# Optimization experiments

Hardware: AMD Instinct MI355X
Metric: run time of the kernel (lower is better)

## Reference

```python
import jax, jax.numpy as jnp
import numpy as np

HIDDEN = 1280
HEADS = 16
HEAD_DIM = HIDDEN // HEADS  # 80
B, N = 2, 2048


def _rotate_half(x):
    half = x.shape[-1] // 2
    return jnp.concatenate([-x[..., half:], x[..., :half]], axis=-1)


def setup_inputs() -> dict:
    key = jax.random.key(0)
    ks = jax.random.split(key, 7)
    x = jax.random.normal(ks[0], (B, N, HIDDEN), dtype=jnp.float32)
    cos = jax.random.uniform(ks[1], (N, HEAD_DIM), dtype=jnp.float32)
    sin = jax.random.uniform(ks[2], (N, HEAD_DIM), dtype=jnp.float32)
    s = 1.0 / np.sqrt(HIDDEN)
    qkv_w = jax.random.normal(ks[3], (HIDDEN, 3 * HIDDEN), dtype=jnp.float32) * s
    qkv_b = jax.random.normal(ks[4], (3 * HIDDEN,), dtype=jnp.float32) * 0.02
    proj_w = jax.random.normal(ks[5], (HIDDEN, HIDDEN), dtype=jnp.float32) * s
    proj_b = jax.random.normal(ks[6], (HIDDEN,), dtype=jnp.float32) * 0.02
    return {"x": x, "cos": cos, "sin": sin, "qkv_w": qkv_w, "qkv_b": qkv_b,
            "proj_w": proj_w, "proj_b": proj_b}


def reference(x, cos, sin, qkv_w, qkv_b, proj_w, proj_b):
    b, n, _ = x.shape
    scale = 1.0 / np.sqrt(HEAD_DIM).astype(np.float32)
    # fused QKV projection
    qkv = x @ qkv_w + qkv_b                                # [b, n, 3*hidden]
    qkv = qkv.reshape(b, n, 3, HEADS, HEAD_DIM)
    qkv = jnp.transpose(qkv, (2, 0, 3, 1, 4))              # [3, b, h, n, hd]
    q, k, v = qkv[0], qkv[1], qkv[2]
    # 2D RoPE
    cos_b = cos[None, None, :, :]
    sin_b = sin[None, None, :, :]
    q = q * cos_b + _rotate_half(q) * sin_b
    k = k * cos_b + _rotate_half(k) * sin_b
    # manual softmax attention
    scores = jnp.einsum('bhqd,bhkd->bhqk', q, k) * scale   # [b, h, n, n]
    attn = jax.nn.softmax(scores, axis=-1)
    out = jnp.einsum('bhqk,bhkd->bhqd', attn, v)           # [b, h, n, hd]
    out = jnp.transpose(out, (0, 2, 1, 3)).reshape(b, n, HIDDEN)
    return out @ proj_w + proj_b
```

## Files before the change

kernel.cpp:

```cpp
#include <hip/hip_runtime.h>
#include <hip/hip_bf16.h>
#include <math.h>

#define HIDDEN 1280
#define HEADS 16
#define HD 80
#define HALF 40
#define BB 2
#define NN 2048
#define MROWS (BB * NN)
#define QSCALE ((float)(0.11180339887498949 * 1.4426950408889634))

typedef __attribute__((ext_vector_type(8))) _Float16 f16x8;
typedef __attribute__((ext_vector_type(4))) float f32x4;

#define AS1 __attribute__((address_space(1)))
#define AS3 __attribute__((address_space(3)))

__device__ __forceinline__ void splitf16(float x, ushort& hi, ushort& lo) {
    _Float16 h = (_Float16)x;
    _Float16 l = (_Float16)(x - (float)h);
    hi = __builtin_bit_cast(ushort, h);
    lo = __builtin_bit_cast(ushort, l);
}

__device__ __forceinline__ ushort f2h(float x) {
    _Float16 h = (_Float16)x;
    return __builtin_bit_cast(ushort, h);
}

__global__ __launch_bounds__(256) void split_f16_kernel(
    const float* __restrict__ in, ushort* __restrict__ hi,
    ushort* __restrict__ lo, int n4)
{
    int i = blockIdx.x * 256 + threadIdx.x;
    if (i >= n4) return;
    float4 v = ((const float4*)in)[i];
    ushort4 h, l;
    splitf16(v.x, h.x, l.x);
    splitf16(v.y, h.y, l.y);
    splitf16(v.z, h.z, l.z);
    splitf16(v.w, h.w, l.w);
    ((ushort4*)hi)[i] = h;
    ((ushort4*)lo)[i] = l;
}

__global__ __launch_bounds__(256) void tsplit_f16_kernel(
    const float* __restrict__ W, ushort* __restrict__ T, int K, int N)
{
    __shared__ float s[32][33];
    const int n0 = blockIdx.x * 32;
    const int k0 = blockIdx.y * 32;
    {
        int tn = threadIdx.x & 31, tk = threadIdx.x >> 5;
        #pragma unroll
        for (int i = 0; i < 4; ++i)
            s[tk + i * 8][tn] = W[(size_t)(k0 + tk + i * 8) * N + n0 + tn];
    }
    __syncthreads();
    {
        int tk = threadIdx.x & 31, tn = threadIdx.x >> 5;
        #pragma unroll
        for (int i = 0; i < 4; ++i)
            T[(size_t)(n0 + tn + i * 8) * K + k0 + tk] = f2h(s[tk][tn + i * 8]);
    }
}

#define BM 128
#define BN 128
#define BK 32

__global__ __launch_bounds__(256) void gemm_f16x2_kernel(
    const ushort* __restrict__ Ahi, const ushort* __restrict__ Alo,
    const ushort* __restrict__ Bh,
    const float* __restrict__ bias, float* __restrict__ C,
    int M, int N, int K)
{
    __shared__ __align__(16) ushort lds[3 * 128 * 32];

    const int tid = threadIdx.x;
    const int wid = tid >> 6;
    const int lane = tid & 63;
    const int col0 = blockIdx.x * BN;
    const int row0 = blockIdx.y * BM;
    const int wy = wid >> 1, wx = wid & 1;
    const int lrow = lane >> 2;
    const int lchunk = lane & 3;

    f32x4 acc[4][4] = {};

    for (int k0 = 0; k0 < K; k0 += BK) {
        __syncthreads();
        #pragma unroll
        for (int i = 0; i < 6; ++i) {
            int s = wid + i * 4;
            int tile = s >> 3, t = s & 7;
            const ushort* src = (tile == 0) ? Ahi : (tile == 1) ? Alo : Bh;
            int srow = (tile < 2) ? row0 : col0;
            const ushort* g = src + (size_t)(srow + t * 16 + lrow) * K + k0 + lchunk * 8;
            ushort* l = lds + tile * 4096 + t * 512 + lane * 8;
            __builtin_amdgcn_global_load_lds(
                (const AS1 unsigned int*)g, (AS3 unsigned int*)l, 16, 0, 0);
        }
        __syncthreads();

        const int q = lane >> 4;
        const int r = lane & 15;
        f16x8 ah[4], al[4], bf[4];
        #pragma unroll
        for (int i = 0; i < 4; ++i) {
            int arow = wy * 64 + i * 16 + r;
            ah[i] = *(const f16x8*)(lds + 0 * 4096 + arow * 32 + q * 8);
            al[i] = *(const f16x8*)(lds + 1 * 4096 + arow * 32 + q * 8);
            int brow = wx * 64 + i * 16 + r;
            bf[i] = *(const f16x8*)(lds + 2 * 4096 + brow * 32 + q * 8);
        }
        #pragma unroll
        for (int i = 0; i < 4; ++i) {
            #pragma unroll
            for (int j = 0; j < 4; ++j) {
                acc[i][j] = __builtin_amdgcn_mfma_f32_16x16x32_f16(al[i], bf[j], acc[i][j], 0, 0, 0);
                acc[i][j] = __builtin_amdgcn_mfma_f32_16x16x32_f16(ah[i], bf[j], acc[i][j], 0, 0, 0);
            }
        }
    }

    const int q = lane >> 4, r = lane & 15;
    #pragma unroll
    for (int i = 0; i < 4; ++i) {
        #pragma unroll
        for (int j = 0; j < 4; ++j) {
            int col = col0 + wx * 64 + j * 16 + r;
            float b = bias[col];
            #pragma unroll
            for (int v = 0; v < 4; ++v) {
                int row = row0 + wy * 64 + i * 16 + q * 4 + v;
                C[(size_t)row * N + col] = acc[i][j][v] + b;
            }
        }
    }
}

__global__ __launch_bounds__(512, 2) void gemm_f16x2_256_kernel(
    const ushort* __restrict__ Ahi, const ushort* __restrict__ Alo,
    const ushort* __restrict__ Bh,
    const float* __restrict__ bias, float* __restrict__ C,
    int M, int N, int K, int nbx)
{
    __shared__ __align__(16) ushort lds[3 * 3 * 8192];

    const int tid = threadIdx.x;
    const int wid = tid >> 6;
    const int lane = tid & 63;
    const int q = lane >> 4, r = lane & 15;
    const int wr = wid >> 2, wc = wid & 3;

    int id = blockIdx.x;
    {
        int nwg = gridDim.x;
        if ((nwg & 7) == 0) {
            int c = nwg >> 3;
            id = (id & 7) * c + (id >> 3);
        }
    }
    const int row0 = (id / nbx) * 256;
    const int col0 = (id % nbx) * 256;

    const ushort* gsrc[6];
    int ldst[6];
    #pragma unroll
    for (int j = 0; j < 6; ++j) {
        int pj = j >> 1;
        int rloc = wid * 32 + (j & 1) * 16 + (lane >> 2);
        int sl = (lane & 3) ^ ((rloc >> 1) & 3);
        const ushort* base = (pj == 0) ? Ahi : (pj == 1) ? Alo : Bh;
        int grow = ((pj < 2) ? row0 : col0) + rloc;
        gsrc[j] = base + (size_t)grow * K + sl * 8;
        ldst[j] = pj * 8192 + (wid * 32 + (j & 1) * 16) * 32 + lane * 8;
    }

    const int NT = K / 32;

    #pragma unroll
    for (int j = 0; j < 6; ++j)
        __builtin_amdgcn_global_load_lds((const AS1 unsigned int*)(gsrc[j]),
            (AS3 unsigned int*)(lds + ldst[j]), 16, 0, 0);
    #pragma unroll
    for (int j = 0; j < 6; ++j)
        __builtin_amdgcn_global_load_lds((const AS1 unsigned int*)(gsrc[j] + 32),
            (AS3 unsigned int*)(lds + 24576 + ldst[j]), 16, 0, 0);
    asm volatile("s_waitcnt vmcnt(6)" ::: "memory");
    __builtin_amdgcn_s_barrier();

    const int soff = (q ^ ((r >> 1) & 3)) * 8;
    const int arow0 = wr * 128 + r;
    const int brow0 = wc * 64 + r;

    f32x4 acc[8][4] = {};
    f16x8 ah[4], al[4], bf[4];

    int cb = 0;
    int nb = 49152;

    for (int t = 0; t < NT; ++t) {
        const ushort* A0 = lds + cb;
        const ushort* A1 = lds + cb + 8192;
        const ushort* Bp = lds + cb + 16384;
        ushort* nbuf = lds + nb;
        const bool st = (t + 2 < NT);
        const int ko = (t + 2) * 32;

        #pragma unroll
        for (int m = 0; m < 4; ++m) {
            int ro = (arow0 + m * 16) * 32 + soff;
            ah[m] = *(const f16x8*)(A0 + ro);
            al[m] = *(const f16x8*)(A1 + ro);
        }
        #pragma unroll
        for (int n = 0; n < 2; ++n)
            bf[n] = *(const f16x8*)(Bp + (brow0 + n * 16) * 32 + soff);
        if (st) {
            __builtin_amdgcn_global_load_lds((const AS1 unsigned int*)(gsrc[0] + ko),
                (AS3 unsigned int*)(nbuf + ldst[0]), 16, 0, 0);
            __builtin_amdgcn_global_load_lds((const AS1 unsigned int*)(gsrc[1] + ko),
                (AS3 unsigned int*)(nbuf + ldst[1]), 16, 0, 0);
        }
        __builtin_amdgcn_s_barrier();
        asm volatile("s_waitcnt lgkmcnt(0)" ::: "memory");
        __builtin_amdgcn_sched_barrier(0);
        __builtin_amdgcn_s_setprio(1);
        #pragma unroll
        for (int m = 0; m < 4; ++m) {
            #pragma unroll
            for (int n = 0; n < 2; ++n) {
                acc[m][n] = __builtin_amdgcn_mfma_f32_16x16x32_f16(al[m], bf[n], acc[m][n], 0, 0, 0);
                acc[m][n] = __builtin_amdgcn_mfma_f32_16x16x32_f16(ah[m], bf[n], acc[m][n], 0, 0, 0);
            }
        }
        __builtin_amdgcn_s_setprio(0);
        __builtin_amdgcn_s_barrier();

        #pragma unroll
        for (int n = 2; n < 4; ++n)
            bf[n] = *(const f16x8*)(Bp + (brow0 + n * 16) * 32 + soff);
        if (st) {
            __builtin_amdgcn_global_load_lds((const AS1 unsigned int*)(gsrc[2] + ko),
                (AS3 unsigned int*)(nbuf + ldst[2]), 16, 0, 0);
            __builtin_amdgcn_global_load_lds((const AS1 unsigned int*)(gsrc[3] + ko),
                (AS3 unsigned int*)(nbuf + ldst[3]), 16, 0, 0);
        }
        __builtin_amdgcn_s_barrier();
        asm volatile("s_waitcnt lgkmcnt(0)" ::: "memory");
        __builtin_amdgcn_sched_barrier(0);
        __builtin_amdgcn_s_setprio(1);
        #pragma unroll
        for (int m = 0; m < 4; ++m) {
            #pragma unroll
            for (int n = 2; n < 4; ++n) {
                acc[m][n] = __builtin_amdgcn_mfma_f32_16x16x32_f16(al[m], bf[n], acc[m][n], 0, 0, 0);
                acc[m][n] = __builtin_amdgcn_mfma_f32_16x16x32_f16(ah[m], bf[n], acc[m][n], 0, 0, 0);
            }
        }
        __builtin_amdgcn_s_setprio(0);
        __builtin_amdgcn_s_barrier();

        #pragma unroll
        for (int m = 0; m < 4; ++m) {
            int ro = (arow0 + (m + 4) * 16) * 32 + soff;
            ah[m] = *(const f16x8*)(A0 + ro);
            al[m] = *(const f16x8*)(A1 + ro);
        }
        if (st) {
            __builtin_amdgcn_global_load_lds((const AS1 unsigned int*)(gsrc[4] + ko),
                (AS3 unsigned int*)(nbuf + ldst[4]), 16, 0, 0);
            __builtin_amdgcn_global_load_lds((const AS1 unsigned int*)(gsrc[5] + ko),
                (AS3 unsigned int*)(nbuf + ldst[5]), 16, 0, 0);
        }
        __builtin_amdgcn_s_barrier();
        asm volatile("s_waitcnt lgkmcnt(0)" ::: "memory");
        __builtin_amdgcn_sched_barrier(0);
        __builtin_amdgcn_s_setprio(1);
        #pragma unroll
        for (int m = 0; m < 4; ++m) {
            #pragma unroll
            for (int n = 2; n < 4; ++n) {
                acc[m + 4][n] = __builtin_amdgcn_mfma_f32_16x16x32_f16(al[m], bf[n], acc[m + 4][n], 0, 0, 0);
                acc[m + 4][n] = __builtin_amdgcn_mfma_f32_16x16x32_f16(ah[m], bf[n], acc[m + 4][n], 0, 0, 0);
            }
        }
        __builtin_amdgcn_s_setprio(0);
        __builtin_amdgcn_s_barrier();

        __builtin_amdgcn_s_setprio(1);
        #pragma unroll
        for (int m = 0; m < 4; ++m) {
            #pragma unroll
            for (int n = 0; n < 2; ++n) {
                acc[m + 4][n] = __builtin_amdgcn_mfma_f32_16x16x32_f16(al[m], bf[n], acc[m + 4][n], 0, 0, 0);
                acc[m + 4][n] = __builtin_amdgcn_mfma_f32_16x16x32_f16(ah[m], bf[n], acc[m + 4][n], 0, 0, 0);
            }
        }
        __builtin_amdgcn_s_setprio(0);
        if (st)
            asm volatile("s_waitcnt vmcnt(6)" ::: "memory");
        else if (t + 1 < NT)
            asm volatile("s_waitcnt vmcnt(0)" ::: "memory");
        __builtin_amdgcn_s_barrier();

        cb += 24576; if (cb == 73728) cb = 0;
        nb += 24576; if (nb == 73728) nb = 0;
    }

    #pragma unroll
    for (int m = 0; m < 8; ++m) {
        #pragma unroll
        for (int n = 0; n < 4; ++n) {
            int col = col0 + wc * 64 + n * 16 + r;
            float b = bias[col];
            #pragma unroll
            for (int v = 0; v < 4; ++v) {
                int row = row0 + wr * 128 + m * 16 + q * 4 + v;
                C[(size_t)row * N + col] = acc[m][n][v] + b;
            }
        }
    }
}

__global__ __launch_bounds__(256) void rope_split_kernel(
    const float* __restrict__ qkv, const float* __restrict__ cos_t,
    const float* __restrict__ sin_t,
    ushort* __restrict__ qf, ushort* __restrict__ kf,
    ushort* __restrict__ vt)
{
    __shared__ float s_v[64][84];
    const int tid = threadIdx.x;
    const int b = blockIdx.z, h = blockIdx.y;
    const int n0 = blockIdx.x * 64;
    const int bh = b * HEADS + h;

    #pragma unroll
    for (int i = 0; i < 5; ++i) {
        int u = tid + i * 256;
        int n = u / 20, c = u % 20;
        const float* src = qkv + (size_t)(b * NN + n0 + n) * 3840 + 2 * HIDDEN + h * HD + c * 4;
        *(float4*)(&s_v[n][c * 4]) = *(const float4*)src;
    }

    for (int u = tid; u < 640; u += 256) {
        int n = u / 10, p = u % 10;
        int d = p * 4;
        int ng = n0 + n;
        size_t rowb = (size_t)(b * NN + ng) * 3840;
        float4 c0 = *(const float4*)(cos_t + ng * HD + d);
        float4 c1 = *(const float4*)(cos_t + ng * HD + d + HALF);
        float4 s0 = *(const float4*)(sin_t + ng * HD + d);
        float4 s1 = *(const float4*)(sin_t + ng * HD + d + HALF);
        size_t qo = ((size_t)bh * NN + ng) * 96;
        {
            float4 x0 = *(const float4*)(qkv + rowb + h * HD + d);
            float4 x1 = *(const float4*)(qkv + rowb + h * HD + d + HALF);
            ushort4 h4a, h4b;
            h4a.x = f2h((x0.x * c0.x - x1.x * s0.x) * QSCALE);
            h4a.y = f2h((x0.y * c0.y - x1.y * s0.y) * QSCALE);
            h4a.z = f2h((x0.z * c0.z - x1.z * s0.z) * QSCALE);
            h4a.w = f2h((x0.w * c0.w - x1.w * s0.w) * QSCALE);
            h4b.x = f2h((x1.x * c1.x + x0.x * s1.x) * QSCALE);
            h4b.y = f2h((x1.y * c1.y + x0.y * s1.y) * QSCALE);
            h4b.z = f2h((x1.z * c1.z + x0.z * s1.z) * QSCALE);
            h4b.w = f2h((x1.w * c1.w + x0.w * s1.w) * QSCALE);
            *(ushort4*)(qf + qo + d) = h4a;
            *(ushort4*)(qf + qo + d + HALF) = h4b;
        }
        {
            float4 x0 = *(const float4*)(qkv + rowb + HIDDEN + h * HD + d);
            float4 x1 = *(const float4*)(qkv + rowb + HIDDEN + h * HD + d + HALF);
            ushort4 h4a, h4b;
            h4a.x = f2h(x0.x * c0.x - x1.x * s0.x);
            h4a.y = f2h(x0.y * c0.y - x1.y * s0.y);
            h4a.z = f2h(x0.z * c0.z - x1.z * s0.z);
            h4a.w = f2h(x0.w * c0.w - x1.w * s0.w);
            h4b.x = f2h(x1.x * c1.x + x0.x * s1.x);
            h4b.y = f2h(x1.y * c1.y + x0.y * s1.y);
            h4b.z = f2h(x1.z * c1.z + x0.z * s1.z);
            h4b.w = f2h(x1.w * c1.w + x0.w * s1.w);
            *(ushort4*)(kf + qo + d) = h4a;
            *(ushort4*)(kf + qo + d + HALF) = h4b;
        }
    }

    {
        int which = tid >> 7;
        int u = tid & 127;
        int n = u >> 1, part = u & 1;
        size_t o = ((size_t)bh * NN + n0 + n) * 96 + 80 + part * 8;
        uint4 z = {0u, 0u, 0u, 0u};
        if (which == 0) *(uint4*)(qf + o) = z;
        else            *(uint4*)(kf + o) = z;
    }
    __syncthreads();

    for (int u = tid; u < 320; u += 256) {
        int d = u >> 2, nc = u & 3;
        ushort hs[16];
        #pragma unroll
        for (int kk = 0; kk < 16; ++kk)
            hs[kk] = f2h(s_v[nc * 16 + kk][d]);
        size_t o = ((size_t)bh * HD + d) * NN + n0 + nc * 16;
        uint4 w0, w1;
        w0.x = (uint)hs[0] | ((uint)hs[1] << 16);
        w0.y = (uint)hs[2] | ((uint)hs[3] << 16);
        w0.z = (uint)hs[4] | ((uint)hs[5] << 16);
        w0.w = (uint)hs[6] | ((uint)hs[7] << 16);
        w1.x = (uint)hs[8] | ((uint)hs[9] << 16);
        w1.y = (uint)hs[10] | ((uint)hs[11] << 16);
        w1.z = (uint)hs[12] | ((uint)hs[13] << 16);
        w1.w = (uint)hs[14] | ((uint)hs[15] << 16);
        *(uint4*)(vt + o) = w0;
        *(uint4*)(vt + o + 8) = w1;
    }
}

__global__ __launch_bounds__(256, 2) void attn_mfma_kernel(
    const ushort* __restrict__ qf, const ushort* __restrict__ kf,
    const ushort* __restrict__ vt,
    ushort* __restrict__ ao_hi, ushort* __restrict__ ao_lo)
{
    __shared__ __align__(16) ushort lds[20480];
    ushort* k_s = lds;
    _Float16* v_s = (_Float16*)(lds + 6144);
    _Float16* p_s = (_Float16*)(lds + 11264);

    const int tid = threadIdx.x;
    const int wave = tid >> 6, lane = tid & 63;
    const int quad = lane >> 4, r = lane & 15;
    const int b = blockIdx.z, h = blockIdx.y;
    const int bh = b * HEADS + h;
    const int q0 = blockIdx.x * 128;

    f16x8 qfr[2][3];
    #pragma unroll
    for (int mt = 0; mt < 2; ++mt)
        #pragma unroll
        for (int c = 0; c < 3; ++c) {
            size_t o = ((size_t)bh * NN + q0 + wave * 32 + mt * 16 + r) * 96 + c * 32 + quad * 8;
            qfr[mt][c] = *(const f16x8*)(qf + o);
        }

    f32x4 oacc[2][5] = {};
    float l_part[2][4] = {};

    const size_t kb = (size_t)bh * NN * 96;
    const size_t vb = (size_t)bh * HD * NN;

    for (int j0 = 0; j0 < NN; j0 += 64) {
        __syncthreads();
        for (int s = wave; s < 22; s += 4) {
            if (s < 12) {
                int off = s * 512 + lane * 8;
                __builtin_amdgcn_global_load_lds(
                    (const AS1 unsigned int*)(kf + kb + (size_t)j0 * 96 + off),
                    (AS3 unsigned int*)(k_s + off), 16, 0, 0);
            } else {
                int ts = s - 12;
                int off = ts * 512 + lane * 8;
                size_t go = vb + (size_t)(ts * 8 + (lane >> 3)) * NN + j0
                          + (size_t)(((lane & 7) ^ (lane >> 3)) * 8);
                __builtin_amdgcn_global_load_lds(
                    (const AS1 unsigned int*)(vt + go),
                    (AS3 unsigned int*)((ushort*)v_s + off), 16, 0, 0);
            }
        }
        __syncthreads();

        f32x4 sc[2][4] = {};
        #pragma unroll
        for (int jt = 0; jt < 4; ++jt) {
            f16x8 kbf[3];
            int j = jt * 16 + r;
            #pragma unroll
            for (int c = 0; c < 3; ++c)
                kbf[c] = *(const f16x8*)(k_s + j * 96 + c * 32 + quad * 8);
            #pragma unroll
            for (int mt = 0; mt < 2; ++mt)
                #pragma unroll
                for (int c = 0; c < 3; ++c)
                    sc[mt][jt] = __builtin_amdgcn_mfma_f32_16x16x32_f16(qfr[mt][c], kbf[c], sc[mt][jt], 0, 0, 0);
        }

        #pragma unroll
        for (int mt = 0; mt < 2; ++mt) {
            #pragma unroll
            for (int v = 0; v < 4; ++v) {
                float ps = 0.0f;
                #pragma unroll
                for (int jt = 0; jt < 4; ++jt) {
                    float p = __builtin_amdgcn_exp2f(sc[mt][jt][v]);
                    sc[mt][jt][v] = p;
                    ps += p;
                }
                l_part[mt][v] += ps;
            }
            int rowbase = wave * 32 + mt * 16 + quad * 4;
            #pragma unroll
            for (int jt = 0; jt < 4; ++jt) {
                int bks = (jt * 2 + (r >> 3)) ^ (quad << 1);
                #pragma unroll
                for (int v = 0; v < 4; ++v)
                    p_s[(rowbase + v) * 64 + bks * 8 + (r & 7)] = (_Float16)sc[mt][jt][v];
            }
        }

        f16x8 pa[2][2];
        #pragma unroll
        for (int mt = 0; mt < 2; ++mt)
            #pragma unroll
            for (int cc = 0; cc < 2; ++cc) {
                int rowp = wave * 32 + mt * 16 + r;
                int bks = (cc * 4 + quad) ^ (((r >> 2) & 3) << 1);
                pa[mt][cc] = *(const f16x8*)(p_s + rowp * 64 + bks * 8);
            }

        #pragma unroll
        for (int dt = 0; dt < 5; ++dt)
            #pragma unroll
            for (int cc = 0; cc < 2; ++cc) {
                int ck = (cc * 4 + quad) ^ (r & 7);
                f16x8 vbf = *(const f16x8*)(v_s + (dt * 16 + r) * 64 + ck * 8);
                oacc[0][dt] = __builtin_amdgcn_mfma_f32_16x16x32_f16(pa[0][cc], vbf, oacc[0][dt], 0, 0, 0);
                oacc[1][dt] = __builtin_amdgcn_mfma_f32_16x16x32_f16(pa[1][cc], vbf, oacc[1][dt], 0, 0, 0);
            }
    }

    float inv_l[2][4];
    #pragma unroll
    for (int mt = 0; mt < 2; ++mt)
        #pragma unroll
        for (int v = 0; v < 4; ++v) {
            float l = l_part[mt][v];
            l += __shfl_xor(l, 1);
            l += __shfl_xor(l, 2);
            l += __shfl_xor(l, 4);
            l += __shfl_xor(l, 8);
            inv_l[mt][v] = 1.0f / l;
        }

    __syncthreads();
    #pragma unroll
    for (int mt = 0; mt < 2; ++mt)
        #pragma unroll
        for (int v = 0; v < 4; ++v) {
            int row = wave * 32 + mt * 16 + quad * 4 + v;
            #pragma unroll
            for (int dt = 0; dt < 5; ++dt) {
                float o = oacc[mt][dt][v] * inv_l[mt][v];
                ushort hh, ll;
                splitf16(o, hh, ll);
                lds[row * 80 + dt * 16 + r] = hh;
                lds[10240 + row * 80 + dt * 16 + r] = ll;
            }
        }
    __syncthreads();
    {
        size_t gbase = ((size_t)b * NN + q0) * HIDDEN + h * HD;
        #pragma unroll
        for (int i = 0; i < 10; ++i) {
            int u = tid + i * 256;
            int plane = u / 1280, idx = u % 1280;
            int row = idx / 10, part = idx % 10;
            uint4 w = *(const uint4*)(lds + plane * 10240 + idx * 8);
            ushort* dst = (plane ? ao_lo : ao_hi) + gbase + (size_t)row * HIDDEN + part * 8;
            *(uint4*)dst = w;
        }
    }
}

extern "C" void kernel_launch(void* const* d_in, const int* in_sizes, int n_in,
                              void* d_out, int out_size, void* d_ws, size_t ws_size,
                              hipStream_t stream)
{
    const float* x      = (const float*)d_in[0];
    const float* cos_t  = (const float*)d_in[1];
    const float* sin_t  = (const float*)d_in[2];
    const float* qkv_w  = (const float*)d_in[3];
    const float* qkv_b  = (const float*)d_in[4];
    const float* proj_w = (const float*)d_in[5];
    const float* proj_b = (const float*)d_in[6];
    float* out = (float*)d_out;

    char* ws = (char*)d_ws;
    float*  qkv   = (float*)ws;
    ushort* ao_hi = (ushort*)ws;
    ushort* ao_lo = (ushort*)(ws + 10485760);
    ushort* wT    = (ushort*)(ws + 62914560);
    ushort* vt    = (ushort*)(ws + 62914560);
    ushort* a_hi  = (ushort*)(ws + 82575360);
    ushort* a_lo  = (ushort*)(ws + 93061120);
    ushort* q_f   = (ushort*)(ws + 83886080);
    ushort* k_f   = (ushort*)(ws + 96468992);

    split_f16_kernel<<<(MROWS * HIDDEN / 4 + 255) / 256, 256, 0, stream>>>(
        x, a_hi, a_lo, MROWS * HIDDEN / 4);

    tsplit_f16_kernel<<<dim3(3 * HIDDEN / 32, HIDDEN / 32), 256, 0, stream>>>(
        qkv_w, wT, HIDDEN, 3 * HIDDEN);

    gemm_f16x2_256_kernel<<<dim3((MROWS / 256) * (3 * HIDDEN / 256)), 512, 0, stream>>>(
        a_hi, a_lo, wT, qkv_b, qkv, MROWS, 3 * HIDDEN, HIDDEN, 3 * HIDDEN / 256);

    rope_split_kernel<<<dim3(NN / 64, HEADS, BB), 256, 0, stream>>>(
        qkv, cos_t, sin_t, q_f, k_f, vt);

    attn_mfma_kernel<<<dim3(NN / 128, HEADS, BB), 256, 0, stream>>>(
        q_f, k_f, vt, ao_hi, ao_lo);

    tsplit_f16_kernel<<<dim3(HIDDEN / 32, HIDDEN / 32), 256, 0, stream>>>(
        proj_w, wT, HIDDEN, HIDDEN);

    gemm_f16x2_kernel<<<dim3(HIDDEN / BN, MROWS / BM), 256, 0, stream>>>(
        ao_hi, ao_lo, wT, proj_b, out, MROWS, HIDDEN, HIDDEN);
}
```

Baseline: 324.7 us.

## Double-buffer K/V tiles in LDS with async prefetch and swizzled K layout

The attention kernel now double-buffers K and V tiles in LDS, issuing global_load_lds for the next tile before computing on the current one, so memory latency overlaps with MFMA work. K rows are padded to 128 halves with an XOR chunk swizzle to reduce LDS bank conflicts. s_setprio is raised around the MFMA sections. LDS use grows to about 68KB per block, which may reduce occupancy below the two blocks per CU requested by the launch bounds.

```diff
diff --git a/kernel.cpp b/kernel.cpp
--- a/kernel.cpp
+++ b/kernel.cpp
@@ -425,10 +425,8 @@
     const ushort* __restrict__ vt,
     ushort* __restrict__ ao_hi, ushort* __restrict__ ao_lo)
 {
-    __shared__ __align__(16) ushort lds[20480];
-    ushort* k_s = lds;
-    _Float16* v_s = (_Float16*)(lds + 6144);
-    _Float16* p_s = (_Float16*)(lds + 11264);
+    __shared__ __align__(16) ushort lds[34816];
+    _Float16* p_s = (_Float16*)(lds + 26624);
 
     const int tid = threadIdx.x;
     const int wave = tid >> 6, lane = tid & 63;
@@ -437,6 +435,32 @@
     const int bh = b * HEADS + h;
     const int q0 = blockIdx.x * 128;
 
+    const size_t kb = (size_t)bh * NN * 96;
+    const size_t vb = (size_t)bh * HD * NN;
+
+    const ushort* gptr[7];
+    int ldso[7];
+    #pragma unroll
+    for (int i = 0; i < 7; ++i) {
+        int s = wave + i * 4;
+        if (s < 16) {
+            int row = s * 4 + (lane >> 4);
+            int t = lane & 15;
+            int g = t ^ (row & 7);
+            if (g >= 12) g = 0;
+            gptr[i] = kf + kb + (size_t)row * 96 + g * 8;
+            ldso[i] = s * 512 + lane * 8;
+        } else if (s < 26) {
+            int ts = s - 16;
+            gptr[i] = vt + vb + (size_t)(ts * 8 + (lane >> 3)) * NN
+                      + (size_t)(((lane & 7) ^ (lane >> 3)) * 8);
+            ldso[i] = 8192 + ts * 512 + lane * 8;
+        } else {
+            gptr[i] = nullptr;
+            ldso[i] = 0;
+        }
+    }
+
     f16x8 qfr[2][3];
     #pragma unroll
     for (int mt = 0; mt < 2; ++mt)
@@ -449,43 +473,54 @@
     f32x4 oacc[2][5] = {};
     float l_part[2][4] = {};
 
-    const size_t kb = (size_t)bh * NN * 96;
-    const size_t vb = (size_t)bh * HD * NN;
-
+    #pragma unroll
+    for (int i = 0; i < 7; ++i) {
+        int s = wave + i * 4;
+        if (s < 26) {
+            __builtin_amdgcn_global_load_lds((const AS1 unsigned int*)gptr[i],
+                (AS3 unsigned int*)(lds + ldso[i]), 16, 0, 0);
+            gptr[i] += (s < 16) ? 6144 : 64;
+        }
+    }
+    asm volatile("s_waitcnt vmcnt(0)" ::: "memory");
+    __builtin_amdgcn_s_barrier();
+
+    int cur = 0;
     for (int j0 = 0; j0 < NN; j0 += 64) {
-        __syncthreads();
-        for (int s = wave; s < 22; s += 4) {
-            if (s < 12) {
-                int off = s * 512 + lane * 8;
-                __builtin_amdgcn_global_load_lds(
-                    (const AS1 unsigned int*)(kf + kb + (size_t)j0 * 96 + off),
-                    (AS3 unsigned int*)(k_s + off), 16, 0, 0);
-            } else {
-                int ts = s - 12;
-                int off = ts * 512 + lane * 8;
-                size_t go = vb + (size_t)(ts * 8 + (lane >> 3)) * NN + j0
-                          + (size_t)(((lane & 7) ^ (lane >> 3)) * 8);
-                __builtin_amdgcn_global_load_lds(
-                    (const AS1 unsigned int*)(vt + go),
-                    (AS3 unsigned int*)((ushort*)v_s + off), 16, 0, 0);
-            }
-        }
-        __syncthreads();
+        const int nxt = 13312 - cur;
+        if (j0 + 64 < NN) {
+            #pragma unroll
+            for (int i = 0; i < 7; ++i) {
+                int s = wave + i * 4;
+                if (s < 26) {
+                    __builtin_amdgcn_global_load_lds((const AS1 unsigned int*)gptr[i],
+                        (AS3 unsigned int*)(lds + nxt + ldso[i]), 16, 0, 0);
+                    gptr[i] += (s < 16) ? 6144 : 64;
+                }
+            }
+        }
+
+        const ushort* k_s = lds + cur;
+        const _Float16* v_s = (const _Float16*)(lds + cur + 8192);
 
         f32x4 sc[2][4] = {};
+        __builtin_amdgcn_s_setprio(1);
         #pragma unroll
         for (int jt = 0; jt < 4; ++jt) {
             f16x8 kbf[3];
             int j = jt * 16 + r;
             #pragma unroll
-            for (int c = 0; c < 3; ++c)
-                kbf[c] = *(const f16x8*)(k_s + j * 96 + c * 32 + quad * 8);
+            for (int c = 0; c < 3; ++c) {
+                int ch = (c * 4 + quad) ^ (r & 7);
+                kbf[c] = *(const f16x8*)(k_s + j * 128 + ch * 8);
+            }
             #pragma unroll
             for (int mt = 0; mt < 2; ++mt)
                 #pragma unroll
                 for (int c = 0; c < 3; ++c)
                     sc[mt][jt] = __builtin_amdgcn_mfma_f32_16x16x32_f16(qfr[mt][c], kbf[c], sc[mt][jt], 0, 0, 0);
         }
+        __builtin_amdgcn_s_setprio(0);
 
         #pragma unroll
         for (int mt = 0; mt < 2; ++mt) {
@@ -520,6 +555,7 @@
                 pa[mt][cc] = *(const f16x8*)(p_s + rowp * 64 + bks * 8);
             }
 
+        __builtin_amdgcn_s_setprio(1);
         #pragma unroll
         for (int dt = 0; dt < 5; ++dt)
             #pragma unroll
@@ -529,6 +565,11 @@
                 oacc[0][dt] = __builtin_amdgcn_mfma_f32_16x16x32_f16(pa[0][cc], vbf, oacc[0][dt], 0, 0, 0);
                 oacc[1][dt] = __builtin_amdgcn_mfma_f32_16x16x32_f16(pa[1][cc], vbf, oacc[1][dt], 0, 0, 0);
             }
+        __builtin_amdgcn_s_setprio(0);
+
+        asm volatile("s_waitcnt vmcnt(0)" ::: "memory");
+        __builtin_amdgcn_s_barrier();
+        cur = nxt;
     }
 
     float inv_l[2][4];
```

Result: no change. 321.6 us (-0.9%).
